# Performance work log

Hardware: AMD Instinct MI355X
Metric: run time of the kernel (lower is better)

The kernel has to match this reference:

```python
import jax, jax.numpy as jnp
import numpy as np

B, S, DIM, H, FR = 2, 1568, 768, 12, 8  # S = FR * 196 spatial tokens, head_dim = 64


def setup_inputs() -> dict:
    key = jax.random.key(0)
    ks = jax.random.split(key, 8)
    s = 0.02
    return {
        "xq": jax.random.normal(ks[0], (B, S, DIM), jnp.float32),
        "xk": jax.random.normal(ks[1], (B, S, DIM), jnp.float32),
        "Wq": jax.random.normal(ks[2], (DIM, DIM), jnp.float32) * s,
        "Wkv": jax.random.normal(ks[3], (DIM, 2 * DIM), jnp.float32) * s,
        "Wpq": jax.random.normal(ks[4], (DIM, DIM), jnp.float32) * s,
        "Wpkv": jax.random.normal(ks[5], (DIM, 2 * DIM), jnp.float32) * s,
        "Wproj": jax.random.normal(ks[6], (DIM, DIM), jnp.float32) * s,
        "bproj": jnp.zeros((DIM,), jnp.float32),
        "num_frames": FR,
    }


def reference(xq, xk, Wq, Wkv, Wpq, Wpkv, Wproj, bproj, num_frames):
    b, s, dim = xq.shape
    f = num_frames
    n = xk.shape[1] // f          # spatial tokens per frame
    h = H
    d = dim // h
    scale = d ** -0.5

    # stage 1: space attention per frame
    q = (xq @ Wq).reshape(b, s, h, d).transpose(0, 2, 1, 3)            # b h s d
    k, v = jnp.split(xk @ Wkv, 2, axis=-1)
    k = k.reshape(b, f * n, h, d).transpose(0, 2, 1, 3)                # b h m d
    v = v.reshape(b, f * n, h, d).transpose(0, 2, 1, 3)                # b h m d
    qk = jnp.einsum('bhsd,bhmd->bhsm', q, k).reshape(b, h, s, f, n)
    attn = jax.nn.softmax(scale * qk, axis=-1)                         # b h s f n
    vf = v.reshape(b, h, f, n, d)
    x = jnp.einsum('bhsfn,bhfnd->bhsfd', attn, vf)                     # b h s f d
    x = x.transpose(0, 2, 3, 1, 4).reshape(b, s, f, dim)               # b s f (h d)

    # diagonal gather: trajectory token for its own frame
    xg = x.reshape(b, f, n, f, dim)
    x_diag = jnp.diagonal(xg, axis1=1, axis2=3)                        # b n dim f
    x_diag = x_diag.transpose(0, 3, 1, 2).reshape(b, s, dim)           # b (f n) dim

    # stage 2: temporal attention over frames
    q2 = (x_diag @ Wpq).reshape(b, s, h, d).transpose(0, 2, 1, 3) * scale  # b h s d
    k2, v2 = jnp.split(x @ Wpkv, 2, axis=-1)
    k2 = k2.reshape(b, s, f, h, d).transpose(0, 3, 1, 2, 4)            # b h s f d
    v2 = v2.reshape(b, s, f, h, d).transpose(0, 3, 1, 2, 4)
    attn2 = jax.nn.softmax(jnp.einsum('bhsd,bhsfd->bhsf', q2, k2), axis=-1)
    out = jnp.einsum('bhsf,bhsfd->bhsd', attn2, v2)                    # b h s d
    out = out.transpose(0, 2, 1, 3).reshape(b, s, dim) @ Wproj + bproj
    return (out, attn2)
```

## Files before the change

kernel.cpp:

```cpp
#include <hip/hip_runtime.h>

#define BDIM 2
#define SEQ  1568
#define DIM  768
#define NH   12
#define FR   8
#define NTOK 196
#define HD   64
#define MTOT (BDIM*SEQ)
#define M2   (MTOT*FR)

typedef __attribute__((ext_vector_type(8))) short s16x8;
typedef __attribute__((ext_vector_type(4))) float f32x4;
typedef __attribute__((ext_vector_type(16))) float f32x16;
typedef __attribute__((ext_vector_type(4))) int i32x4;

static __device__ __forceinline__ float bf2f(ushort u) {
  return __uint_as_float(((unsigned)u) << 16);
}
static __device__ __forceinline__ ushort f2bf(float f) {
  unsigned u = __float_as_uint(f);
  unsigned r = (u + 0x7fffu + ((u >> 16) & 1u)) >> 16;
  return (ushort)r;
}
static __device__ __forceinline__ f32x4 mfma16(s16x8 a, s16x8 b, f32x4 c) {
  return __builtin_amdgcn_mfma_f32_16x16x32_bf16(a, b, c, 0, 0, 0);
}
static __device__ __forceinline__ f32x16 mfma32(s16x8 a, s16x8 b, f32x16 c) {
  return __builtin_amdgcn_mfma_f32_32x32x16_bf16(a, b, c, 0, 0, 0);
}
static __device__ __forceinline__ int cvtpk(float lo, float hi) {
  int r;
  asm("v_cvt_pk_bf16_f32 %0, %1, %2" : "=v"(r) : "v"(lo), "v"(hi));
  return r;
}
static __device__ __forceinline__ void gload_lds16(const ushort* g, ushort* l) {
  __builtin_amdgcn_global_load_lds(
      (const __attribute__((address_space(1))) void*)g,
      (__attribute__((address_space(3))) void*)l, 16, 0, 0);
}

__global__ __launch_bounds__(256)
void cvt_all(const float* __restrict__ xq, const float* __restrict__ xk,
             ushort* __restrict__ xqbf, ushort* __restrict__ xkbf,
             const float* __restrict__ Wq, const float* __restrict__ Wkv,
             const float* __restrict__ Wpq, const float* __restrict__ Wproj,
             const float* __restrict__ Wpkv,
             ushort* __restrict__ WqT, ushort* __restrict__ WkvT,
             ushort* __restrict__ WpqT, ushort* __restrict__ WprT,
             ushort* __restrict__ WpkvT, int n4) {
  __shared__ float T[64][65];
  const int blk = blockIdx.x;
  const int tid = threadIdx.x;

  if (blk < 4704) {
    int i = blk*256 + tid;
    const float* src; ushort* dst; int j;
    if (i < n4)        { src = xq; dst = xqbf; j = i; }
    else               { src = xk; dst = xkbf; j = i - n4; }
    float4 v = ((const float4*)src)[j];
    ushort4 o; o.x = f2bf(v.x); o.y = f2bf(v.y); o.z = f2bf(v.z); o.w = f2bf(v.w);
    ((ushort4*)dst)[j] = o;
    return;
  }

  int idx = blk - 4704;
  const int wid = idx / 288; idx %= 288;
  const int ky = idx / 24;
  const int nx = idx % 24;
  const float* W; ushort* WT; int N;
  switch (wid) {
    case 0: W = Wq;    WT = WqT;   N = DIM;   break;
    case 1: W = Wkv;   WT = WkvT;  N = 2*DIM; break;
    case 2: W = Wpq;   WT = WpqT;  N = DIM;   break;
    case 3: W = Wproj; WT = WprT;  N = DIM;   break;
    default: W = Wpkv; WT = WpkvT; N = 2*DIM; break;
  }
  if (nx >= N/64) return;
  #pragma unroll
  for (int it = 0; it < 4; it++) {
    int id2 = it*256 + tid;
    int r = id2 >> 4, c4 = (id2 & 15) << 2;
    float4 v = *(const float4*)&W[(size_t)(ky*64 + r)*N + nx*64 + c4];
    T[r][c4+0] = v.x; T[r][c4+1] = v.y; T[r][c4+2] = v.z; T[r][c4+3] = v.w;
  }
  __syncthreads();
  #pragma unroll
  for (int it = 0; it < 4; it++) {
    int id2 = it*256 + tid;
    int n = id2 >> 4, k4 = (id2 & 15) << 2;
    ushort4 o;
    o.x = f2bf(T[k4+0][n]); o.y = f2bf(T[k4+1][n]);
    o.z = f2bf(T[k4+2][n]); o.w = f2bf(T[k4+3][n]);
    *(ushort4*)&WT[(size_t)(nx*64 + n)*DIM + ky*64 + k4] = o;
  }
}

__global__ __launch_bounds__(256)
void vtrans(const ushort* __restrict__ kvbf, ushort* __restrict__ Vt) {
  __shared__ ushort Vl[NTOK][72];
  const int x = blockIdx.x;
  const int h = x % NH, f = (x / NH) % FR, b = x / (NH*FR);
  const int tid = threadIdx.x;
  for (int idx = tid; idx < NTOK*16; idx += 256) {
    int n = idx >> 4, c4 = (idx & 15) << 2;
    const ushort* p = kvbf + (size_t)(b*SEQ + f*NTOK + n)*(2*DIM) + DIM + h*HD + c4;
    *(ushort4*)&Vl[n][c4] = *(const ushort4*)p;
  }
  __syncthreads();
  ushort* vb = Vt + (size_t)x * (HD*224);
  for (int idx = tid; idx < 64*56; idx += 256) {
    int d = idx / 56, n4 = (idx % 56) << 2;
    ushort4 o;
    o.x = (n4+0 < NTOK) ? Vl[n4+0][d] : (ushort)0;
    o.y = (n4+1 < NTOK) ? Vl[n4+1][d] : (ushort)0;
    o.z = (n4+2 < NTOK) ? Vl[n4+2][d] : (ushort)0;
    o.w = (n4+3 < NTOK) ? Vl[n4+3][d] : (ushort)0;
    *(ushort4*)&vb[(size_t)d*224 + n4] = o;
  }
}

__global__ __launch_bounds__(256)
void proj_pair(const ushort* __restrict__ xqbf, const ushort* __restrict__ xkbf,
               const ushort* __restrict__ WqT, const ushort* __restrict__ WkvT,
               ushort* __restrict__ qbf, ushort* __restrict__ kvbf)
{
  __shared__ ushort As[128][32];
  __shared__ ushort Bs[64][32];
  const int bx = blockIdx.x, by = blockIdx.y;
  const ushort* A; const ushort* Bt; ushort* C; int N, col0; float scale;
  if (bx < 12) { A = xqbf; Bt = WqT;  C = qbf;  N = DIM;   col0 = bx*64;      scale = 0.125f; }
  else         { A = xkbf; Bt = WkvT; C = kvbf; N = 2*DIM; col0 = (bx-12)*64; scale = 1.0f; }

  const int tid = threadIdx.x;
  const int w = tid >> 6, lane = tid & 63;
  const int lq = lane & 15, quad = lane >> 4;
  const int lrow = tid >> 2, lcol = (tid & 3) << 3;

  int ar0 = by*128 + lrow;       if (ar0 > MTOT-1) ar0 = MTOT-1;
  int ar1 = by*128 + 64 + lrow;  if (ar1 > MTOT-1) ar1 = MTOT-1;
  const size_t aoff0 = (size_t)ar0*DIM + lcol;
  const size_t aoff1 = (size_t)ar1*DIM + lcol;
  const size_t boff  = (size_t)(col0 + lrow)*DIM + lcol;

  f32x4 acc[2][4] = {};
  for (int k0 = 0; k0 < DIM; k0 += 32) {
    __syncthreads();
    gload_lds16(A  + aoff0 + k0, &As[w*16][0]);
    gload_lds16(A  + aoff1 + k0, &As[64 + w*16][0]);
    gload_lds16(Bt + boff  + k0, &Bs[w*16][0]);
    __syncthreads();
    s16x8 af[2], bw[4];
    #pragma unroll
    for (int i = 0; i < 2; i++) af[i] = *(const s16x8*)&As[w*32 + i*16 + lq][quad*8];
    #pragma unroll
    for (int j = 0; j < 4; j++) bw[j] = *(const s16x8*)&Bs[j*16 + lq][quad*8];
    #pragma unroll
    for (int i = 0; i < 2; i++)
      #pragma unroll
      for (int j = 0; j < 4; j++)
        acc[i][j] = mfma16(af[i], bw[j], acc[i][j]);
  }

  #pragma unroll
  for (int i = 0; i < 2; i++) {
    #pragma unroll
    for (int r = 0; r < 4; r++) {
      int row = by*128 + w*32 + i*16 + quad*4 + r;
      if (row < MTOT) {
        #pragma unroll
        for (int j = 0; j < 4; j++)
          C[(size_t)row*N + col0 + j*16 + lq] = f2bf(acc[i][j][r] * scale);
      }
    }
  }
}

template<bool BIAS, bool DIAG, bool BF16OUT>
__global__ __launch_bounds__(256)
void gemm64(const ushort* __restrict__ A, const ushort* __restrict__ Bt,
            void* __restrict__ Cv, const float* __restrict__ bias,
            int M, int N, float scale)
{
  __shared__ ushort As[128][32];
  __shared__ ushort Bs[64][32];
  const int bx = blockIdx.x, by = blockIdx.y;
  const int tid = threadIdx.x;
  const int w = tid >> 6, lane = tid & 63;
  const int lq = lane & 15, quad = lane >> 4;
  const int lrow = tid >> 2, lcol = (tid & 3) << 3;
  const int col0 = bx*64;

  int ar0 = by*128 + lrow;       if (ar0 > M-1) ar0 = M-1;
  int ar1 = by*128 + 64 + lrow;  if (ar1 > M-1) ar1 = M-1;
  size_t aoff0, aoff1;
  if (DIAG) {
    int f0 = (ar0 % SEQ) / NTOK, f1 = (ar1 % SEQ) / NTOK;
    aoff0 = ((size_t)ar0*FR + f0)*DIM + lcol;
    aoff1 = ((size_t)ar1*FR + f1)*DIM + lcol;
  } else {
    aoff0 = (size_t)ar0*DIM + lcol;
    aoff1 = (size_t)ar1*DIM + lcol;
  }
  const size_t boff = (size_t)(col0 + lrow)*DIM + lcol;

  f32x4 acc[2][4] = {};
  for (int k0 = 0; k0 < DIM; k0 += 32) {
    __syncthreads();
    gload_lds16(A  + aoff0 + k0, &As[w*16][0]);
    gload_lds16(A  + aoff1 + k0, &As[64 + w*16][0]);
    gload_lds16(Bt + boff  + k0, &Bs[w*16][0]);
    __syncthreads();
    s16x8 af[2], bw[4];
    #pragma unroll
    for (int i = 0; i < 2; i++) af[i] = *(const s16x8*)&As[w*32 + i*16 + lq][quad*8];
    #pragma unroll
    for (int j = 0; j < 4; j++) bw[j] = *(const s16x8*)&Bs[j*16 + lq][quad*8];
    #pragma unroll
    for (int i = 0; i < 2; i++)
      #pragma unroll
      for (int j = 0; j < 4; j++)
        acc[i][j] = mfma16(af[i], bw[j], acc[i][j]);
  }

  #pragma unroll
  for (int i = 0; i < 2; i++) {
    #pragma unroll
    for (int r = 0; r < 4; r++) {
      int row = by*128 + w*32 + i*16 + quad*4 + r;
      if (row < M) {
        #pragma unroll
        for (int j = 0; j < 4; j++) {
          int col = col0 + j*16 + lq;
          float v = acc[i][j][r] * scale;
          if (BIAS) v += bias[col];
          if (BF16OUT) ((ushort*)Cv)[(size_t)row*N + col] = f2bf(v);
          else         ((float*)Cv)[(size_t)row*N + col] = v;
        }
      }
    }
  }
}

__global__ __launch_bounds__(256)
void gemm_logits(const ushort* __restrict__ A, const ushort* __restrict__ Bt,
                 float* __restrict__ Lg, const float* __restrict__ q2)
{
  __shared__ ushort As[128][32];
  __shared__ ushort Bs[128][32];
  __shared__ float  q2s[16][128];

  const int tid = threadIdx.x;
  const int by = blockIdx.x, bx = blockIdx.y;
  const int w = tid >> 6, lane = tid & 63;
  const int lq = lane & 15, quad = lane >> 4;
  const int wr = (w >> 1) * 64, wc = (w & 1) * 64;

  const int lrow = tid >> 2, lcol = (tid & 3) << 3;
  const size_t aoff0 = (size_t)(by*128 + lrow)*DIM + lcol;
  const size_t aoff1 = (size_t)(by*128 + 64 + lrow)*DIM + lcol;
  const size_t boff0 = (size_t)(bx*128 + lrow)*DIM + lcol;
  const size_t boff1 = (size_t)(bx*128 + 64 + lrow)*DIM + lcol;

  {
    int tt = tid >> 4, c0 = (tid & 15) << 3;
    const float* src = q2 + (size_t)(by*16 + tt)*DIM + bx*128 + c0;
    *(float4*)&q2s[tt][c0]     = *(const float4*)src;
    *(float4*)&q2s[tt][c0 + 4] = *(const float4*)(src + 4);
  }

  f32x4 acc[4][4] = {};
  for (int k0 = 0; k0 < DIM; k0 += 32) {
    __syncthreads();
    gload_lds16(A  + aoff0 + k0, &As[w*16][0]);
    gload_lds16(A  + aoff1 + k0, &As[64 + w*16][0]);
    gload_lds16(Bt + boff0 + k0, &Bs[w*16][0]);
    gload_lds16(Bt + boff1 + k0, &Bs[64 + w*16][0]);
    __syncthreads();
    s16x8 af[4], bw[4];
    #pragma unroll
    for (int i = 0; i < 4; i++) af[i] = *(const s16x8*)&As[wr + i*16 + lq][quad*8];
    #pragma unroll
    for (int j = 0; j < 4; j++) bw[j] = *(const s16x8*)&Bs[wc + j*16 + lq][quad*8];
    #pragma unroll
    for (int i = 0; i < 4; i++)
      #pragma unroll
      for (int j = 0; j < 4; j++)
        acc[i][j] = mfma16(af[i], bw[j], acc[i][j]);
  }

  const int head = bx*2 + (wc >> 6);
  #pragma unroll
  for (int i = 0; i < 4; i++) {
    #pragma unroll
    for (int r = 0; r < 4; r++) {
      int rl = wr + i*16 + quad*4 + r;
      int tt = rl >> 3;
      float p = 0.f;
      #pragma unroll
      for (int j = 0; j < 4; j++)
        p += acc[i][j][r] * q2s[tt][wc + j*16 + lq];
      p += __shfl_xor(p, 1); p += __shfl_xor(p, 2);
      p += __shfl_xor(p, 4); p += __shfl_xor(p, 8);
      if (lq == 0)
        Lg[(size_t)(by*128 + rl)*NH + head] = p;
    }
  }
}

__global__ __launch_bounds__(256)
void softagg(const float* __restrict__ Lg, const ushort* __restrict__ x,
             float* __restrict__ attn2, ushort* __restrict__ xa)
{
  __shared__ float as[32][NH][FR];
  const int t0 = blockIdx.x * 32;
  const int tid = threadIdx.x;

  for (int idx = tid; idx < 32*NH; idx += 256) {
    int tl = idx / NH, h = idx % NH;
    int gt = t0 + tl;
    const float* lp = Lg + (size_t)(gt*FR)*NH + h;
    float v[FR], m = -1e30f;
    #pragma unroll
    for (int f = 0; f < FR; f++) { v[f] = lp[f*NH]; m = fmaxf(m, v[f]); }
    float s = 0.f;
    #pragma unroll
    for (int f = 0; f < FR; f++) { v[f] = __expf(v[f] - m); s += v[f]; }
    float inv = 1.0f / s;
    int b = gt / SEQ, sI = gt % SEQ;
    float* ao = attn2 + ((size_t)(b*NH + h)*SEQ + sI)*FR;
    #pragma unroll
    for (int f = 0; f < FR; f++) {
      float a = v[f] * inv;
      ao[f] = a; as[tl][h][f] = a;
    }
  }
  __syncthreads();

  for (int idx = tid; idx < 32*96; idx += 256) {
    int tl = idx / 96, c8 = idx % 96;
    int gt = t0 + tl;
    int col = c8*8, h = col >> 6;
    const ushort* xp = x + ((size_t)gt*FR)*DIM + col;
    float av[8] = {};
    #pragma unroll
    for (int f = 0; f < FR; f++) {
      float a = as[tl][h][f];
      s16x8 xv = *(const s16x8*)(xp + (size_t)f*DIM);
      #pragma unroll
      for (int e = 0; e < 8; e++) av[e] += a * bf2f((ushort)xv[e]);
    }
    ushort4 o0, o1;
    o0.x = f2bf(av[0]); o0.y = f2bf(av[1]); o0.z = f2bf(av[2]); o0.w = f2bf(av[3]);
    o1.x = f2bf(av[4]); o1.y = f2bf(av[5]); o1.z = f2bf(av[6]); o1.w = f2bf(av[7]);
    ushort* op = xa + (size_t)gt*DIM + col;
    *(ushort4*)op = o0; *(ushort4*)(op + 4) = o1;
  }
}

__global__ __launch_bounds__(256)
void stage1_mfma(const ushort* __restrict__ qbf, const ushort* __restrict__ kvbf,
                 const ushort* __restrict__ Vt, ushort* __restrict__ x)
{
  __shared__ ushort sh[208*64];

  const int bh = blockIdx.x;
  const int f  = blockIdx.y;
  const int qt = blockIdx.z;
  const int b = bh / NH, h = bh % NH;
  const int tid = threadIdx.x;
  const int w = tid >> 6, lane = tid & 63;
  const int l31 = lane & 31, hl = lane >> 5;

  const ushort* kbase = kvbf + ((size_t)b*SEQ + f*NTOK)*(2*DIM) + h*HD;
  #pragma unroll
  for (int p = 0; p < 6; ++p) {
    const int c = w*6 + p;
    const int row = c*8 + (lane >> 3);
    const ushort* src = kbase + (size_t)row*(2*DIM)
                      + (((lane & 7) ^ (lane >> 3)) << 3);
    gload_lds16(src, &sh[c*512]);
  }
  {
    const int row = 192 + (tid >> 4);
    const int c4  = (tid & 15) << 2;
    ushort4 v; v.x = 0; v.y = 0; v.z = 0; v.w = 0;
    if (row < NTOK)
      v = *(const ushort4*)(kbase + (size_t)row*(2*DIM) + c4);
    *(ushort4*)&sh[row*64 + ((((c4 >> 3) ^ (row & 7)) << 3) | (c4 & 7))] = v;
  }

  int qrow = qt*128 + w*32 + l31; if (qrow > SEQ-1) qrow = SEQ-1;
  const ushort* qp = qbf + ((size_t)b*SEQ + qrow)*DIM + h*HD + hl*8;
  const s16x8 bq0 = *(const s16x8*)(qp);
  const s16x8 bq1 = *(const s16x8*)(qp + 16);
  const s16x8 bq2 = *(const s16x8*)(qp + 32);
  const s16x8 bq3 = *(const s16x8*)(qp + 48);

  __syncthreads();

  f32x16 acc[7];
  {
    f32x16 z = {};
    #pragma unroll
    for (int nt = 0; nt < 7; ++nt) acc[nt] = z;
  }
  const int sx = l31 & 7;
  #pragma unroll
  for (int nt = 0; nt < 7; ++nt) {
    const int rl = (nt == 6) ? (l31 & 15) : l31;
    const int rbase = (nt*32 + rl)*64;
    acc[nt] = mfma32(*(const s16x8*)&sh[rbase + (((0 + hl) ^ sx) << 3)], bq0, acc[nt]);
    acc[nt] = mfma32(*(const s16x8*)&sh[rbase + (((2 + hl) ^ sx) << 3)], bq1, acc[nt]);
    acc[nt] = mfma32(*(const s16x8*)&sh[rbase + (((4 + hl) ^ sx) << 3)], bq2, acc[nt]);
    acc[nt] = mfma32(*(const s16x8*)&sh[rbase + (((6 + hl) ^ sx) << 3)], bq3, acc[nt]);
  }

  __syncthreads();

  float s0 = 0.f, s1 = 0.f, s2 = 0.f, s3 = 0.f;
  #pragma unroll
  for (int nt = 0; nt < 7; ++nt) {
    #pragma unroll
    for (int g = 0; g < 16; ++g) {
      float e;
      if (nt == 6) {
        if (g < 4) { e = __expf(acc[6][g]); if (hl) e = 0.f; }
        else e = 0.f;
      } else {
        e = __expf(acc[nt][g]);
      }
      acc[nt][g] = e;
      if ((g & 3) == 0) s0 += e; else if ((g & 3) == 1) s1 += e;
      else if ((g & 3) == 2) s2 += e; else s3 += e;
    }
  }
  float sum = (s0 + s1) + (s2 + s3);
  sum += __shfl_xor(sum, 32);
  const float sinv = 1.0f / sum;

  f32x16 o0, o1;
  { f32x16 z = {}; o0 = z; o1 = z; }
  const ushort* vb = Vt + ((size_t)((b*FR + f)*NH + h)) * (HD*224);
  const ushort* vr0 = vb + (size_t)l31*224 + hl*8;
  const ushort* vr1 = vr0 + 32*224;
  #pragma unroll
  for (int nt = 0; nt < 7; ++nt) {
    #pragma unroll
    for (int kh = 0; kh < 2; ++kh) {
      int w0 = cvtpk(acc[nt][8*kh+0], acc[nt][8*kh+1]);
      int w1 = cvtpk(acc[nt][8*kh+2], acc[nt][8*kh+3]);
      int w2 = cvtpk(acc[nt][8*kh+4], acc[nt][8*kh+5]);
      int w3 = cvtpk(acc[nt][8*kh+6], acc[nt][8*kh+7]);
      asm("v_permlane32_swap_b32 %0, %1" : "+v"(w0), "+v"(w2));
      asm("v_permlane32_swap_b32 %0, %1" : "+v"(w1), "+v"(w3));
      union { i32x4 i; s16x8 s; } u;
      u.i.x = w0; u.i.y = w1; u.i.z = w2; u.i.w = w3;
      const int ks = nt*2 + kh;
      const s16x8 va0 = *(const s16x8*)(vr0 + ks*16);
      const s16x8 va1 = *(const s16x8*)(vr1 + ks*16);
      o0 = mfma32(va0, u.s, o0);
      o1 = mfma32(va1, u.s, o1);
    }
  }

  ushort* XT = sh + w*2048;
  #pragma unroll
  for (int dt = 0; dt < 2; ++dt) {
    #pragma unroll
    for (int c = 0; c < 4; ++c) {
      #pragma unroll
      for (int rp = 0; rp < 2; ++rp) {
        const float lo = (dt ? o1[4*c + 2*rp]     : o0[4*c + 2*rp])     * sinv;
        const float hi = (dt ? o1[4*c + 2*rp + 1] : o0[4*c + 2*rp + 1]) * sinv;
        const int word = cvtpk(lo, hi);
        const int d = dt*32 + 8*c + 4*hl + 2*rp;
        *(uint*)&XT[l31*64 + (((d >> 3) ^ (l31 & 7)) << 3) + (d & 7)] = (uint)word;
      }
    }
  }
  #pragma unroll
  for (int it = 0; it < 4; ++it) {
    const int q = it*8 + (lane >> 3);
    const int g = lane & 7;
    s16x8 xv = *(const s16x8*)&XT[q*64 + ((g ^ (q & 7)) << 3)];
    const int s = qt*128 + w*32 + q;
    if (s < SEQ) {
      ushort* xp = x + (((size_t)b*SEQ + s)*FR + f)*DIM + h*HD + g*8;
      *(s16x8*)xp = xv;
    }
  }
}

extern "C" void kernel_launch(void* const* d_in, const int* in_sizes, int n_in,
                              void* d_out, int out_size, void* d_ws, size_t ws_size,
                              hipStream_t stream) {
  const float* xq    = (const float*)d_in[0];
  const float* xk    = (const float*)d_in[1];
  const float* Wq    = (const float*)d_in[2];
  const float* Wkv   = (const float*)d_in[3];
  const float* Wpq   = (const float*)d_in[4];
  const float* Wpkv  = (const float*)d_in[5];
  const float* Wproj = (const float*)d_in[6];
  const float* bproj = (const float*)d_in[7];

  float* out   = (float*)d_out;
  float* attn2 = out + (size_t)MTOT*DIM;

  ushort* ws    = (ushort*)d_ws;
  ushort* xbf   = ws;
  ushort* kvbf  = xbf + (size_t)MTOT*FR*DIM;
  float*  q2    = (float*)kvbf;
  ushort* qbf   = kvbf + (size_t)MTOT*2*DIM;
  ushort* zbf   = qbf;
  ushort* xqbf  = qbf + (size_t)MTOT*DIM;
  ushort* xkbf  = xqbf + (size_t)MTOT*DIM;
  ushort* Vt    = xqbf;
  float*  Lg    = (float*)xqbf;
  ushort* xa    = xkbf;
  ushort* WqT   = xkbf + (size_t)MTOT*DIM;
  ushort* WkvT  = WqT  + (size_t)DIM*DIM;
  ushort* WpqT  = WkvT + (size_t)2*DIM*DIM;
  ushort* WprT  = WpqT + (size_t)DIM*DIM;
  ushort* WpkvT = WprT + (size_t)DIM*DIM;

  dim3 blk(256);
  const int n4 = MTOT*DIM/4;

  cvt_all<<<dim3(4704 + 1440), blk, 0, stream>>>(
      xq, xk, xqbf, xkbf, Wq, Wkv, Wpq, Wproj, Wpkv,
      WqT, WkvT, WpqT, WprT, WpkvT, n4);

  proj_pair<<<dim3(36, (MTOT+127)/128), blk, 0, stream>>>(
      xqbf, xkbf, WqT, WkvT, qbf, kvbf);
  vtrans<<<dim3(BDIM*FR*NH), blk, 0, stream>>>(kvbf, Vt);
  stage1_mfma<<<dim3(BDIM*NH, FR, (SEQ+127)/128), blk, 0, stream>>>(qbf, kvbf, Vt, xbf);
  gemm64<false,true,false><<<dim3(12, (MTOT+127)/128), blk, 0, stream>>>(
      xbf, WpqT, q2, nullptr, MTOT, DIM, 0.125f);
  gemm_logits<<<dim3(M2/128, 6), blk, 0, stream>>>(xbf, WpkvT, Lg, q2);
  softagg<<<dim3(MTOT/32), blk, 0, stream>>>(Lg, xbf, attn2, xa);
  gemm64<false,false,true><<<dim3(12, (MTOT+127)/128), blk, 0, stream>>>(
      xa, WpkvT + (size_t)DIM*DIM, zbf, nullptr, MTOT, DIM, 1.0f);
  gemm64<true,false,false><<<dim3(12, (MTOT+127)/128), blk, 0, stream>>>(
      zbf, WprT, out, bproj, MTOT, DIM, 1.0f);
}
```

Measured before the change: 273.0 us.

## Reassociate temporal logits via q·Wk and fold Wv into output projection

Instead of projecting every per-frame token through Wpk (an M2 x 768 x 768 GEMM) and then dotting with q2, the code first computes q2 times Wk transposed per head (qw), then takes dot products of qw with the raw stage-1 outputs x. This is done in three 256-channel chunks that accumulate partial logits. The V projection and the output projection are also merged into one precomputed combined weight (Wpv·Wproj), which removes a full GEMM over all tokens. The extra costs are a small weight-product GEMM per call, an extra bf16 rounding of the combined weight and of q2, and several additional small kernel launches.

```diff
diff --git a/kernel.cpp b/kernel.cpp
--- a/kernel.cpp
+++ b/kernel.cpp
@@ -48,7 +48,8 @@
              const float* __restrict__ Wpkv,
              ushort* __restrict__ WqT, ushort* __restrict__ WkvT,
              ushort* __restrict__ WpqT, ushort* __restrict__ WprT,
-             ushort* __restrict__ WpkvT, int n4) {
+             ushort* __restrict__ Wpk_bf, ushort* __restrict__ Wpv_bf,
+             int n4) {
   __shared__ float T[64][65];
   const int blk = blockIdx.x;
   const int tid = threadIdx.x;
@@ -64,35 +65,49 @@
     return;
   }
 
-  int idx = blk - 4704;
-  const int wid = idx / 288; idx %= 288;
-  const int ky = idx / 24;
-  const int nx = idx % 24;
-  const float* W; ushort* WT; int N;
-  switch (wid) {
-    case 0: W = Wq;    WT = WqT;   N = DIM;   break;
-    case 1: W = Wkv;   WT = WkvT;  N = 2*DIM; break;
-    case 2: W = Wpq;   WT = WpqT;  N = DIM;   break;
-    case 3: W = Wproj; WT = WprT;  N = DIM;   break;
-    default: W = Wpkv; WT = WpkvT; N = 2*DIM; break;
-  }
-  if (nx >= N/64) return;
-  #pragma unroll
-  for (int it = 0; it < 4; it++) {
-    int id2 = it*256 + tid;
-    int r = id2 >> 4, c4 = (id2 & 15) << 2;
-    float4 v = *(const float4*)&W[(size_t)(ky*64 + r)*N + nx*64 + c4];
-    T[r][c4+0] = v.x; T[r][c4+1] = v.y; T[r][c4+2] = v.z; T[r][c4+3] = v.w;
-  }
-  __syncthreads();
-  #pragma unroll
-  for (int it = 0; it < 4; it++) {
-    int id2 = it*256 + tid;
-    int n = id2 >> 4, k4 = (id2 & 15) << 2;
-    ushort4 o;
-    o.x = f2bf(T[k4+0][n]); o.y = f2bf(T[k4+1][n]);
-    o.z = f2bf(T[k4+2][n]); o.w = f2bf(T[k4+3][n]);
-    *(ushort4*)&WT[(size_t)(nx*64 + n)*DIM + ky*64 + k4] = o;
+  if (blk < 5856) {
+    int idx = blk - 4704;
+    const int wid = idx / 288; idx %= 288;
+    const int ky = idx / 24;
+    const int nx = idx % 24;
+    const float* W; ushort* WT; int N;
+    switch (wid) {
+      case 0: W = Wq;    WT = WqT;   N = DIM;   break;
+      case 1: W = Wkv;   WT = WkvT;  N = 2*DIM; break;
+      case 2: W = Wpq;   WT = WpqT;  N = DIM;   break;
+      default: W = Wproj; WT = WprT; N = DIM;   break;
+    }
+    if (nx >= N/64) return;
+    #pragma unroll
+    for (int it = 0; it < 4; it++) {
+      int id2 = it*256 + tid;
+      int r = id2 >> 4, c4 = (id2 & 15) << 2;
+      float4 v = *(const float4*)&W[(size_t)(ky*64 + r)*N + nx*64 + c4];
+      T[r][c4+0] = v.x; T[r][c4+1] = v.y; T[r][c4+2] = v.z; T[r][c4+3] = v.w;
+    }
+    __syncthreads();
+    #pragma unroll
+    for (int it = 0; it < 4; it++) {
+      int id2 = it*256 + tid;
+      int n = id2 >> 4, k4 = (id2 & 15) << 2;
+      ushort4 o;
+      o.x = f2bf(T[k4+0][n]); o.y = f2bf(T[k4+1][n]);
+      o.z = f2bf(T[k4+2][n]); o.w = f2bf(T[k4+3][n]);
+      *(ushort4*)&WT[(size_t)(nx*64 + n)*DIM + ky*64 + k4] = o;
+    }
+    return;
+  }
+
+  {
+    int id2 = blk - 5856;
+    int half = id2 / 576;
+    int e = (id2 % 576)*256 + tid;
+    int r = e / 192;
+    int c4 = (e % 192) * 4;
+    float4 v = *(const float4*)&Wpkv[(size_t)r*(2*DIM) + half*DIM + c4];
+    ushort4 o; o.x = f2bf(v.x); o.y = f2bf(v.y); o.z = f2bf(v.z); o.w = f2bf(v.w);
+    ushort* dst = half ? Wpv_bf : Wpk_bf;
+    *(ushort4*)&dst[(size_t)r*DIM + c4] = o;
   }
 }
 
@@ -243,67 +258,106 @@
 }
 
 __global__ __launch_bounds__(256)
-void gemm_logits(const ushort* __restrict__ A, const ushort* __restrict__ Bt,
-                 float* __restrict__ Lg, const float* __restrict__ q2)
+void qwgemm(const ushort* __restrict__ q2bf, const ushort* __restrict__ Wpk,
+            ushort* __restrict__ qw, int j)
 {
   __shared__ ushort As[128][32];
-  __shared__ ushort Bs[128][32];
-  __shared__ float  q2s[16][128];
-
-  const int tid = threadIdx.x;
-  const int by = blockIdx.x, bx = blockIdx.y;
+  __shared__ ushort Bs[64][32];
+  const int bx = blockIdx.x, by = blockIdx.y;
+  const int h = bx >> 2, ct = bx & 3;
+  const int tid = threadIdx.x;
   const int w = tid >> 6, lane = tid & 63;
   const int lq = lane & 15, quad = lane >> 4;
-  const int wr = (w >> 1) * 64, wc = (w & 1) * 64;
-
   const int lrow = tid >> 2, lcol = (tid & 3) << 3;
-  const size_t aoff0 = (size_t)(by*128 + lrow)*DIM + lcol;
-  const size_t aoff1 = (size_t)(by*128 + 64 + lrow)*DIM + lcol;
-  const size_t boff0 = (size_t)(bx*128 + lrow)*DIM + lcol;
-  const size_t boff1 = (size_t)(bx*128 + 64 + lrow)*DIM + lcol;
-
-  {
-    int tt = tid >> 4, c0 = (tid & 15) << 3;
-    const float* src = q2 + (size_t)(by*16 + tt)*DIM + bx*128 + c0;
-    *(float4*)&q2s[tt][c0]     = *(const float4*)src;
-    *(float4*)&q2s[tt][c0 + 4] = *(const float4*)(src + 4);
-  }
-
-  f32x4 acc[4][4] = {};
-  for (int k0 = 0; k0 < DIM; k0 += 32) {
+
+  int ar0 = by*128 + lrow;       if (ar0 > MTOT-1) ar0 = MTOT-1;
+  int ar1 = by*128 + 64 + lrow;  if (ar1 > MTOT-1) ar1 = MTOT-1;
+  const size_t aoff0 = (size_t)ar0*DIM + h*HD + lcol;
+  const size_t aoff1 = (size_t)ar1*DIM + h*HD + lcol;
+  const size_t boff  = (size_t)(j*256 + ct*64 + lrow)*DIM + h*HD + lcol;
+
+  f32x4 acc[2][4] = {};
+  #pragma unroll
+  for (int k0 = 0; k0 < 64; k0 += 32) {
     __syncthreads();
-    gload_lds16(A  + aoff0 + k0, &As[w*16][0]);
-    gload_lds16(A  + aoff1 + k0, &As[64 + w*16][0]);
-    gload_lds16(Bt + boff0 + k0, &Bs[w*16][0]);
-    gload_lds16(Bt + boff1 + k0, &Bs[64 + w*16][0]);
+    gload_lds16(q2bf + aoff0 + k0, &As[w*16][0]);
+    gload_lds16(q2bf + aoff1 + k0, &As[64 + w*16][0]);
+    gload_lds16(Wpk  + boff  + k0, &Bs[w*16][0]);
     __syncthreads();
-    s16x8 af[4], bw[4];
-    #pragma unroll
-    for (int i = 0; i < 4; i++) af[i] = *(const s16x8*)&As[wr + i*16 + lq][quad*8];
-    #pragma unroll
-    for (int j = 0; j < 4; j++) bw[j] = *(const s16x8*)&Bs[wc + j*16 + lq][quad*8];
-    #pragma unroll
-    for (int i = 0; i < 4; i++)
+    s16x8 af[2], bw[4];
+    #pragma unroll
+    for (int i = 0; i < 2; i++) af[i] = *(const s16x8*)&As[w*32 + i*16 + lq][quad*8];
+    #pragma unroll
+    for (int jj = 0; jj < 4; jj++) bw[jj] = *(const s16x8*)&Bs[jj*16 + lq][quad*8];
+    #pragma unroll
+    for (int i = 0; i < 2; i++)
       #pragma unroll
-      for (int j = 0; j < 4; j++)
-        acc[i][j] = mfma16(af[i], bw[j], acc[i][j]);
-  }
-
-  const int head = bx*2 + (wc >> 6);
-  #pragma unroll
-  for (int i = 0; i < 4; i++) {
+      for (int jj = 0; jj < 4; jj++)
+        acc[i][jj] = mfma16(af[i], bw[jj], acc[i][jj]);
+  }
+
+  #pragma unroll
+  for (int i = 0; i < 2; i++) {
     #pragma unroll
     for (int r = 0; r < 4; r++) {
-      int rl = wr + i*16 + quad*4 + r;
-      int tt = rl >> 3;
-      float p = 0.f;
-      #pragma unroll
-      for (int j = 0; j < 4; j++)
-        p += acc[i][j][r] * q2s[tt][wc + j*16 + lq];
-      p += __shfl_xor(p, 1); p += __shfl_xor(p, 2);
-      p += __shfl_xor(p, 4); p += __shfl_xor(p, 8);
-      if (lq == 0)
-        Lg[(size_t)(by*128 + rl)*NH + head] = p;
+      int row = by*128 + w*32 + i*16 + quad*4 + r;
+      if (row < MTOT) {
+        #pragma unroll
+        for (int jj = 0; jj < 4; jj++) {
+          int cl = ct*64 + jj*16 + lq;
+          qw[(size_t)row*(NH*256) + h*256 + cl] = f2bf(acc[i][jj][r]);
+        }
+      }
+    }
+  }
+}
+
+template<bool FIRST>
+__global__ __launch_bounds__(256)
+void fplogits(const ushort* __restrict__ qw, const ushort* __restrict__ x,
+              float* __restrict__ Lp, int c0)
+{
+  __shared__ ushort xs[4*8*264];
+  __shared__ ushort qws[4*12*264];
+  const int tid = threadIdx.x;
+  const int t0 = blockIdx.x * 4;
+
+  #pragma unroll
+  for (int r = 0; r < 4; ++r) {
+    int id = r*256 + tid;
+    int tt = id >> 8, f = (id >> 5) & 7, ch = id & 31;
+    s16x8 v = *(const s16x8*)(x + ((size_t)(t0+tt)*FR + f)*DIM + c0 + ch*8);
+    *(s16x8*)&xs[(tt*8 + f)*264 + ch*8] = v;
+  }
+  #pragma unroll
+  for (int r = 0; r < 6; ++r) {
+    int id = r*256 + tid;
+    int tt = id / 384, rem = id % 384;
+    int h = rem >> 5, ch = rem & 31;
+    s16x8 v = *(const s16x8*)(qw + (size_t)(t0+tt)*(NH*256) + h*256 + ch*8);
+    *(s16x8*)&qws[(tt*12 + h)*264 + ch*8] = v;
+  }
+  __syncthreads();
+
+  const int w = tid >> 6, lane = tid & 63;
+  const int lq = lane & 15, quad = lane >> 4;
+  const int fr = lq & 7;
+  const int hc = (lq < 12) ? lq : 0;
+  f32x4 acc = {};
+  #pragma unroll
+  for (int k0 = 0; k0 < 256; k0 += 32) {
+    s16x8 a = *(const s16x8*)&xs[(w*8 + fr)*264 + quad*8 + k0];
+    s16x8 b = *(const s16x8*)&qws[(w*12 + hc)*264 + quad*8 + k0];
+    acc = mfma16(a, b, acc);
+  }
+
+  if (quad < 2 && lq < 12) {
+    float* lp = Lp + (size_t)(t0 + w)*96 + lq;
+    #pragma unroll
+    for (int r = 0; r < 4; ++r) {
+      int f = quad*4 + r;
+      if (FIRST) lp[f*NH] = acc[r];
+      else       lp[f*NH] += acc[r];
     }
   }
 }
@@ -507,40 +561,52 @@
   float* out   = (float*)d_out;
   float* attn2 = out + (size_t)MTOT*DIM;
 
-  ushort* ws    = (ushort*)d_ws;
-  ushort* xbf   = ws;
-  ushort* kvbf  = xbf + (size_t)MTOT*FR*DIM;
-  float*  q2    = (float*)kvbf;
-  ushort* qbf   = kvbf + (size_t)MTOT*2*DIM;
-  ushort* zbf   = qbf;
-  ushort* xqbf  = qbf + (size_t)MTOT*DIM;
-  ushort* xkbf  = xqbf + (size_t)MTOT*DIM;
-  ushort* Vt    = xqbf;
-  float*  Lg    = (float*)xqbf;
-  ushort* xa    = xkbf;
-  ushort* WqT   = xkbf + (size_t)MTOT*DIM;
-  ushort* WkvT  = WqT  + (size_t)DIM*DIM;
-  ushort* WpqT  = WkvT + (size_t)2*DIM*DIM;
-  ushort* WprT  = WpqT + (size_t)DIM*DIM;
-  ushort* WpkvT = WprT + (size_t)DIM*DIM;
+  ushort* ws     = (ushort*)d_ws;
+  ushort* xbf    = ws;
+  ushort* kvbf   = xbf + (size_t)MTOT*FR*DIM;
+  ushort* q2bf   = kvbf;
+  ushort* qbf    = kvbf + (size_t)MTOT*2*DIM;
+  ushort* xqbf   = qbf + (size_t)MTOT*DIM;
+  ushort* xkbf   = xqbf + (size_t)MTOT*DIM;
+  ushort* Vt     = xqbf;
+  float*  Lp     = (float*)xqbf;
+  ushort* xa     = xkbf;
+  ushort* WqT    = xkbf + (size_t)MTOT*DIM;
+  ushort* WkvT   = WqT  + (size_t)DIM*DIM;
+  ushort* WpqT   = WkvT + (size_t)2*DIM*DIM;
+  ushort* WprT   = WpqT + (size_t)DIM*DIM;
+  ushort* Wpk_bf = WprT + (size_t)DIM*DIM;
+  ushort* Wpv_bf = Wpk_bf + (size_t)DIM*DIM;
+  ushort* WcombT = Wpv_bf + (size_t)DIM*DIM;
+  ushort* qw     = WcombT + (size_t)DIM*DIM;
 
   dim3 blk(256);
   const int n4 = MTOT*DIM/4;
 
-  cvt_all<<<dim3(4704 + 1440), blk, 0, stream>>>(
+  cvt_all<<<dim3(4704 + 1152 + 1152), blk, 0, stream>>>(
       xq, xk, xqbf, xkbf, Wq, Wkv, Wpq, Wproj, Wpkv,
-      WqT, WkvT, WpqT, WprT, WpkvT, n4);
+      WqT, WkvT, WpqT, WprT, Wpk_bf, Wpv_bf, n4);
+
+  gemm64<false,false,true><<<dim3(12, 6), blk, 0, stream>>>(
+      WprT, Wpv_bf, WcombT, nullptr, DIM, DIM, 1.0f);
 
   proj_pair<<<dim3(36, (MTOT+127)/128), blk, 0, stream>>>(
       xqbf, xkbf, WqT, WkvT, qbf, kvbf);
   vtrans<<<dim3(BDIM*FR*NH), blk, 0, stream>>>(kvbf, Vt);
   stage1_mfma<<<dim3(BDIM*NH, FR, (SEQ+127)/128), blk, 0, stream>>>(qbf, kvbf, Vt, xbf);
-  gemm64<false,true,false><<<dim3(12, (MTOT+127)/128), blk, 0, stream>>>(
-      xbf, WpqT, q2, nullptr, MTOT, DIM, 0.125f);
-  gemm_logits<<<dim3(M2/128, 6), blk, 0, stream>>>(xbf, WpkvT, Lg, q2);
-  softagg<<<dim3(MTOT/32), blk, 0, stream>>>(Lg, xbf, attn2, xa);
-  gemm64<false,false,true><<<dim3(12, (MTOT+127)/128), blk, 0, stream>>>(
-      xa, WpkvT + (size_t)DIM*DIM, zbf, nullptr, MTOT, DIM, 1.0f);
+
+  gemm64<false,true,true><<<dim3(12, (MTOT+127)/128), blk, 0, stream>>>(
+      xbf, WpqT, q2bf, nullptr, MTOT, DIM, 0.125f);
+
+  qwgemm<<<dim3(48, 25), blk, 0, stream>>>(q2bf, Wpk_bf, qw, 0);
+  fplogits<true><<<dim3(MTOT/4), blk, 0, stream>>>(qw, xbf, Lp, 0);
+  qwgemm<<<dim3(48, 25), blk, 0, stream>>>(q2bf, Wpk_bf, qw, 1);
+  fplogits<false><<<dim3(MTOT/4), blk, 0, stream>>>(qw, xbf, Lp, 256);
+  qwgemm<<<dim3(48, 25), blk, 0, stream>>>(q2bf, Wpk_bf, qw, 2);
+  fplogits<false><<<dim3(MTOT/4), blk, 0, stream>>>(qw, xbf, Lp, 512);
+
+  softagg<<<dim3(MTOT/32), blk, 0, stream>>>(Lp, xbf, attn2, xa);
+
   gemm64<true,false,false><<<dim3(12, (MTOT+127)/128), blk, 0, stream>>>(
-      zbf, WprT, out, bproj, MTOT, DIM, 1.0f);
-}
+      xa, WcombT, out, bproj, MTOT, DIM, 1.0f);
+}
```

New measurement: 273.0 us. No clear change (+0.0%).
